# Optimization experiments

Hardware: AMD Instinct MI355X
Metric: run time of the kernel (lower is better)

Reference implementation:

```python
import jax, jax.numpy as jnp
import numpy as np

B, T, C, H = 2, 2048, 2048, 16
HD = C // H  # head dim = 128
BASE = 10000.0


def _rope_tables(seq_len, d):
    p = jnp.arange(d // 2, dtype=jnp.float32)
    # faithful to source: exponent uses 2**p (power of two), not 2*p
    theta = jnp.power(BASE, -(2.0 ** p) / d)            # [d/2]
    pos = jnp.arange(1, seq_len + 1, dtype=jnp.float32)[:, None]  # 1-indexed positions
    c = pos * theta                                      # [T, d/2]
    ang = jnp.concatenate([c, c], axis=-1)               # [T, d]
    return jnp.cos(ang), jnp.sin(ang)


def _rope(x):
    # x: [B, H, T, d]
    d = x.shape[-1]
    cos, sin = _rope_tables(x.shape[-2], d)
    half = d // 2
    x_rot = jnp.concatenate([-x[..., half:], x[..., :half]], axis=-1)
    return x * cos + x_rot * sin


def setup_inputs() -> dict:
    key = jax.random.key(0)
    k1, k2, k3 = jax.random.split(key, 3)
    x = jax.random.normal(k1, (B, T, C), dtype=jnp.float32)
    Wqkv = jax.random.normal(k2, (3 * C, C), dtype=jnp.float32) * 0.02
    bqkv = jnp.zeros((3 * C,), dtype=jnp.float32)
    Wo = jax.random.normal(k3, (C, C), dtype=jnp.float32) * 0.02
    bo = jnp.zeros((C,), dtype=jnp.float32)
    return {"x": x, "Wqkv": Wqkv, "bqkv": bqkv, "Wo": Wo, "bo": bo}


def reference(x, Wqkv, bqkv, Wo, bo):
    b, t, c = x.shape
    qkv = x @ Wqkv.T + bqkv                      # [B, T, 3C]
    q, k, v = jnp.split(qkv, 3, axis=-1)
    # [B, T, C] -> [B, H, T, HD]
    def to_heads(z):
        return z.reshape(b, t, H, HD).transpose(0, 2, 1, 3)
    q, k, v = to_heads(q), to_heads(k), to_heads(v)
    q = _rope(q)
    k = _rope(k)
    scale = 1.0 / jnp.sqrt(jnp.float32(HD))
    att = jnp.einsum('bhqd,bhkd->bhqk', q, k) * scale   # [B, H, T, T]
    causal = jnp.tril(jnp.ones((t, t), dtype=bool))
    att = jnp.where(causal, att, -jnp.inf)
    att = jax.nn.softmax(att, axis=-1)
    y = jnp.einsum('bhqk,bhkd->bhqd', att, v)           # [B, H, T, HD]
    y = y.transpose(0, 2, 1, 3).reshape(b, t, c)
    y = y @ Wo.T + bo
    return y
```

## Files before the change

### kernel.cpp

```cpp
#include <hip/hip_runtime.h>
#include <hip/hip_bf16.h>


typedef __attribute__((ext_vector_type(8))) short short8;
typedef __attribute__((ext_vector_type(4))) float f32x4;

#define B_  2
#define T_  2048
#define C_  2048
#define H_  16
#define HD_ 128

__device__ __forceinline__ float bf2f(unsigned short u) {
  union { unsigned int i; float f; } v; v.i = ((unsigned int)u) << 16; return v.f;
}
__device__ __forceinline__ unsigned short f2bf(float f) {
  union { float f; unsigned int i; } v; v.f = f;
  unsigned int x = v.i;
  return (unsigned short)((x + 0x7fffu + ((x >> 16) & 1u)) >> 16);
}
__device__ __forceinline__ float fexp2(float x) {
#if __has_builtin(__builtin_amdgcn_exp2f)
  return __builtin_amdgcn_exp2f(x);
#else
  return exp2f(x);
#endif
}

__device__ __forceinline__ void gll16(const unsigned short* g, unsigned short* lds_base) {
  __builtin_amdgcn_global_load_lds(
      (const __attribute__((address_space(1))) void*)g,
      (__attribute__((address_space(3))) void*)lds_base, 16, 0, 0);
}

__global__ void cvt_k(const float* __restrict__ src, unsigned short* __restrict__ dst, int n4)
{
  int i = blockIdx.x * blockDim.x + threadIdx.x;
  if (i < n4) {
    float4 v = ((const float4*)src)[i];
    ushort4 h;
    h.x = f2bf(v.x); h.y = f2bf(v.y); h.z = f2bf(v.z); h.w = f2bf(v.w);
    ((ushort4*)dst)[i] = h;
  }
}

template<int MODE>
__global__ __launch_bounds__(256, 2)
void gemm_bt(const unsigned short* __restrict__ A,
             const unsigned short* __restrict__ Bw,
             const float* __restrict__ bias,
             float* __restrict__ Cout,
             unsigned short* __restrict__ Qb,
             unsigned short* __restrict__ Kb,
             unsigned short* __restrict__ Vb,
             int N, int K)
{
  __shared__ unsigned short Al[128 * 64];
  __shared__ unsigned short Bl[128 * 64];
  const int tid  = threadIdx.x;
  const int wave = tid >> 6, lane = tid & 63;
  const int quad = lane >> 4, l15 = lane & 15;
  const int wm = wave >> 1, wn = wave & 1;
  const int n0 = blockIdx.x * 128, m0 = blockIdx.y * 128;

  f32x4 acc[4][4];
#pragma unroll
  for (int i = 0; i < 4; i++)
#pragma unroll
    for (int j = 0; j < 4; j++) acc[i][j] = (f32x4){0.f, 0.f, 0.f, 0.f};

  for (int k0 = 0; k0 < K; k0 += 64) {
    __syncthreads();
    const unsigned short* Ag = A + (size_t)m0 * K + k0;
    const unsigned short* Bg = Bw + (size_t)n0 * K + k0;
#pragma unroll
    for (int i = 0; i < 4; i++) {
      int cc = i * 256 + wave * 64 + lane;
      int r = cc >> 3;
      int c8 = (cc & 7) ^ (r & 7);
      gll16(Ag + (size_t)r * K + c8 * 8, &Al[(i * 4 + wave) * 512]);
      gll16(Bg + (size_t)r * K + c8 * 8, &Bl[(i * 4 + wave) * 512]);
    }
    __syncthreads();
#pragma unroll
    for (int kc = 0; kc < 2; kc++) {
      const int csw = (((kc * 4 + quad) ^ (l15 & 7)) * 8);
      short8 af[4], bfr[4];
#pragma unroll
      for (int mi = 0; mi < 4; mi++)
        af[mi] = *(const short8*)&Al[(wm * 64 + mi * 16 + l15) * 64 + csw];
#pragma unroll
      for (int ni = 0; ni < 4; ni++)
        bfr[ni] = *(const short8*)&Bl[(wn * 64 + ni * 16 + l15) * 64 + csw];
#pragma unroll
      for (int mi = 0; mi < 4; mi++)
#pragma unroll
        for (int ni = 0; ni < 4; ni++)
          acc[mi][ni] = __builtin_amdgcn_mfma_f32_16x16x32_bf16(af[mi], bfr[ni], acc[mi][ni], 0, 0, 0);
    }
  }

  if constexpr (MODE == 0) {
#pragma unroll
    for (int mi = 0; mi < 4; mi++)
#pragma unroll
      for (int ni = 0; ni < 4; ni++) {
        int col = n0 + wn * 64 + ni * 16 + l15;
        float bv = bias[col];
#pragma unroll
        for (int r = 0; r < 4; r++) {
          int row = m0 + wm * 64 + mi * 16 + quad * 4 + r;
          Cout[(size_t)row * N + col] = acc[mi][ni][r] + bv;
        }
      }
  } else {
    int which = n0 >> 11;
    int h = (n0 >> 7) & 15;
    unsigned short* P = (which == 0) ? Qb : (which == 1) ? Kb : Vb;
#pragma unroll
    for (int mi = 0; mi < 4; mi++)
#pragma unroll
      for (int ni = 0; ni < 4; ni++) {
        int d = wn * 64 + ni * 16 + l15;
        float bv = bias[n0 + d];
#pragma unroll
        for (int r = 0; r < 4; r++) {
          int m = m0 + wm * 64 + mi * 16 + quad * 4 + r;
          int b = m >> 11, t = m & (T_ - 1);
          size_t addr = (which == 2)
              ? ((size_t)((b * H_ + h) * HD_ + d)) * T_ + t
              : ((size_t)((b * H_ + h) * T_ + t)) * HD_ + d;
          P[addr] = f2bf(acc[mi][ni][r] + bv);
        }
      }
  }
}

__global__ void rope_k(unsigned short* __restrict__ Q, unsigned short* __restrict__ K)
{
  const int tid = threadIdx.x;
  const int w = tid >> 6, l = tid & 63;
  const int r = blockIdx.x * 4 + w;
  const int t = r & (T_ - 1);
  const float pos = (float)(t + 1);
  const float theta = expf(-exp2f((float)l) * 0.07195578415606394f);
  const float ang = pos * theta;
  const float c = cosf(ang), s = sinf(ang);
  const float QS = 0.08838834764831845f * 1.4426950408889634f;
  const size_t base = (size_t)r * HD_;

  float q0 = bf2f(Q[base + l]), q1 = bf2f(Q[base + l + 64]);
  Q[base + l]      = f2bf((q0 * c - q1 * s) * QS);
  Q[base + l + 64] = f2bf((q1 * c + q0 * s) * QS);
  float k0 = bf2f(K[base + l]), k1 = bf2f(K[base + l + 64]);
  K[base + l]      = f2bf(k0 * c - k1 * s);
  K[base + l + 64] = f2bf(k1 * c + k0 * s);
}

__global__ __launch_bounds__(256, 2)
void attn_k(const unsigned short* __restrict__ Q,
            const unsigned short* __restrict__ K,
            const unsigned short* __restrict__ Vt_g,
            unsigned short* __restrict__ AO)
{
  __shared__ unsigned short Kl[64 * 128];
  __shared__ unsigned short Vl[128 * 64];
  __shared__ unsigned short Pl[4 * 16 * 72];

  const int tid  = threadIdx.x;
  const int wave = tid >> 6, lane = tid & 63;
  const int quad = lane >> 4, l15 = lane & 15;
  const int blk = blockIdx.x;
  const int bh = (blk & 7) + 8 * ((blk >> 3) & 3);
  const int qp = (blk >> 5) & 15;
  const unsigned short* Qh = Q    + (size_t)bh * T_ * HD_;
  const unsigned short* Kh = K    + (size_t)bh * T_ * HD_;
  const unsigned short* Vh = Vt_g + (size_t)bh * T_ * HD_;
  const int b = bh >> 4, h = bh & 15;

#pragma unroll
  for (int tile = 0; tile < 2; tile++) {
    const int q0 = (tile == 0 ? qp : 31 - qp) * 64;
    const int wq = q0 + wave * 16;
    short8 qf[4];
#pragma unroll
    for (int kc = 0; kc < 4; kc++)
      qf[kc] = *(const short8*)&Qh[(size_t)(wq + l15) * HD_ + kc * 32 + quad * 8];

    f32x4 oacc[8];
#pragma unroll
    for (int n = 0; n < 8; n++) oacc[n] = (f32x4){0.f, 0.f, 0.f, 0.f};
    float mst[4], lst[4];
#pragma unroll
    for (int r = 0; r < 4; r++) { mst[r] = -1e30f; lst[r] = 0.f; }

    const int niter = (q0 >> 6) + 1;
    for (int it = 0; it < niter; it++) {
      const int kt = it * 64;
      __syncthreads();
#pragma unroll
      for (int i = 0; i < 4; i++) {
        int cc = i * 256 + wave * 64 + lane;
        int kr = cc >> 4, kcs = (cc & 15) ^ (kr & 15);
        gll16(Kh + (size_t)(kt + kr) * HD_ + kcs * 8, &Kl[(i * 4 + wave) * 512]);
        int vr = cc >> 3, vcs = (cc & 7) ^ (vr & 7);
        gll16(Vh + (size_t)vr * T_ + kt + vcs * 8, &Vl[(i * 4 + wave) * 512]);
      }
      __syncthreads();

      f32x4 sa[4];
#pragma unroll
      for (int ni = 0; ni < 4; ni++) sa[ni] = (f32x4){0.f, 0.f, 0.f, 0.f};
#pragma unroll
      for (int kc = 0; kc < 4; kc++) {
        const int cswK = (((kc * 4 + quad) ^ l15) * 8);
        short8 bfr[4];
#pragma unroll
        for (int ni = 0; ni < 4; ni++)
          bfr[ni] = *(const short8*)&Kl[(ni * 16 + l15) * HD_ + cswK];
#pragma unroll
        for (int ni = 0; ni < 4; ni++)
          sa[ni] = __builtin_amdgcn_mfma_f32_16x16x32_bf16(qf[kc], bfr[ni], sa[ni], 0, 0, 0);
      }

      if (kt == q0) {
#pragma unroll
        for (int ni = 0; ni < 4; ni++) {
          int gcol = kt + ni * 16 + l15;
#pragma unroll
          for (int r = 0; r < 4; r++) {
            int grow = wq + quad * 4 + r;
            if (gcol > grow) sa[ni][r] = -1e30f;
          }
        }
      }

      float rmax[4] = {-1e30f, -1e30f, -1e30f, -1e30f};
#pragma unroll
      for (int ni = 0; ni < 4; ni++)
#pragma unroll
        for (int r = 0; r < 4; r++) rmax[r] = fmaxf(rmax[r], sa[ni][r]);
#pragma unroll
      for (int r = 0; r < 4; r++)
#pragma unroll
        for (int off = 1; off < 16; off <<= 1)
          rmax[r] = fmaxf(rmax[r], __shfl_xor(rmax[r], off));
      float alpha[4];
#pragma unroll
      for (int r = 0; r < 4; r++) {
        float mnew = fmaxf(mst[r], rmax[r]);
        alpha[r] = fexp2(fminf(mst[r] - mnew, 0.f));
        mst[r] = mnew;
      }
      float rsum[4] = {0.f, 0.f, 0.f, 0.f};
#pragma unroll
      for (int ni = 0; ni < 4; ni++)
#pragma unroll
        for (int r = 0; r < 4; r++) {
          float p = fexp2(fminf(sa[ni][r] - mst[r], 0.f));
          sa[ni][r] = p;
          rsum[r] += p;
        }
#pragma unroll
      for (int r = 0; r < 4; r++) {
#pragma unroll
        for (int off = 1; off < 16; off <<= 1)
          rsum[r] += __shfl_xor(rsum[r], off);
        lst[r] = lst[r] * alpha[r] + rsum[r];
      }
#pragma unroll
      for (int nv = 0; nv < 8; nv++)
#pragma unroll
        for (int r = 0; r < 4; r++) oacc[nv][r] *= alpha[r];
#pragma unroll
      for (int ni = 0; ni < 4; ni++)
#pragma unroll
        for (int r = 0; r < 4; r++)
          Pl[wave * 16 * 72 + (quad * 4 + r) * 72 + ni * 16 + l15] = f2bf(sa[ni][r]);
      __syncthreads();

      short8 pf[2];
#pragma unroll
      for (int kc = 0; kc < 2; kc++)
        pf[kc] = *(const short8*)&Pl[wave * 16 * 72 + l15 * 72 + kc * 32 + quad * 8];
#pragma unroll
      for (int kc = 0; kc < 2; kc++) {
        const int cswV = (((kc * 4 + quad) ^ (l15 & 7)) * 8);
#pragma unroll
        for (int nv = 0; nv < 8; nv++) {
          short8 vb = *(const short8*)&Vl[(nv * 16 + l15) * 64 + cswV];
          oacc[nv] = __builtin_amdgcn_mfma_f32_16x16x32_bf16(pf[kc], vb, oacc[nv], 0, 0, 0);
        }
      }
    }

    float linv[4];
#pragma unroll
    for (int r = 0; r < 4; r++) linv[r] = 1.0f / fmaxf(lst[r], 1e-20f);
#pragma unroll
    for (int nv = 0; nv < 8; nv++)
#pragma unroll
      for (int r = 0; r < 4; r++) {
        int t = wq + quad * 4 + r;
        int d = nv * 16 + l15;
        AO[((size_t)(b * T_ + t)) * C_ + h * HD_ + d] = f2bf(oacc[nv][r] * linv[r]);
      }
  }
}

template<int A32, int B32, int MODE>
__global__ __launch_bounds__(256, 2)
void gemm_nt(const void* __restrict__ Ap, const void* __restrict__ Bp,
             const float* __restrict__ bias,
             float* __restrict__ Cout,
             unsigned short* __restrict__ Qb,
             unsigned short* __restrict__ Kb,
             unsigned short* __restrict__ Vb,
             int N, int K)
{
  __shared__ unsigned short Al[128 * 72];
  __shared__ unsigned short Bl[128 * 72];
  const int tid  = threadIdx.x;
  const int wave = tid >> 6, lane = tid & 63;
  const int quad = lane >> 4, l15 = lane & 15;
  const int wm = wave >> 1, wn = wave & 1;
  const int n0 = blockIdx.x * 128, m0 = blockIdx.y * 128;

  f32x4 acc[4][4];
#pragma unroll
  for (int i = 0; i < 4; i++)
#pragma unroll
    for (int j = 0; j < 4; j++) acc[i][j] = (f32x4){0.f, 0.f, 0.f, 0.f};

  for (int k0 = 0; k0 < K; k0 += 64) {
    __syncthreads();
    if constexpr (A32) {
      const float* A = (const float*)Ap;
#pragma unroll
      for (int i = 0; i < 8; i++) {
        int cid = tid + i * 256;
        int r = cid >> 4, c = cid & 15;
        float4 v = *(const float4*)&A[(size_t)(m0 + r) * K + k0 + c * 4];
        ushort4 hh;
        hh.x = f2bf(v.x); hh.y = f2bf(v.y); hh.z = f2bf(v.z); hh.w = f2bf(v.w);
        *(ushort4*)&Al[r * 72 + c * 4] = hh;
      }
    } else {
      const unsigned short* A = (const unsigned short*)Ap;
#pragma unroll
      for (int i = 0; i < 4; i++) {
        int cid = tid + i * 256;
        int r = cid >> 3, c = cid & 7;
        *(float4*)&Al[r * 72 + c * 8] =
            *(const float4*)&A[(size_t)(m0 + r) * K + k0 + c * 8];
      }
    }
    if constexpr (B32) {
      const float* Bm = (const float*)Bp;
#pragma unroll
      for (int i = 0; i < 8; i++) {
        int cid = tid + i * 256;
        int r = cid >> 4, c = cid & 15;
        float4 v = *(const float4*)&Bm[(size_t)(n0 + r) * K + k0 + c * 4];
        ushort4 hh;
        hh.x = f2bf(v.x); hh.y = f2bf(v.y); hh.z = f2bf(v.z); hh.w = f2bf(v.w);
        *(ushort4*)&Bl[r * 72 + c * 4] = hh;
      }
    } else {
      const unsigned short* Bm = (const unsigned short*)Bp;
#pragma unroll
      for (int i = 0; i < 4; i++) {
        int cid = tid + i * 256;
        int r = cid >> 3, c = cid & 7;
        *(float4*)&Bl[r * 72 + c * 8] =
            *(const float4*)&Bm[(size_t)(n0 + r) * K + k0 + c * 8];
      }
    }
    __syncthreads();
#pragma unroll
    for (int kc = 0; kc < 2; kc++) {
      short8 af[4], bfr[4];
#pragma unroll
      for (int mi = 0; mi < 4; mi++)
        af[mi] = *(const short8*)&Al[(wm * 64 + mi * 16 + l15) * 72 + kc * 32 + quad * 8];
#pragma unroll
      for (int ni = 0; ni < 4; ni++)
        bfr[ni] = *(const short8*)&Bl[(wn * 64 + ni * 16 + l15) * 72 + kc * 32 + quad * 8];
#pragma unroll
      for (int mi = 0; mi < 4; mi++)
#pragma unroll
        for (int ni = 0; ni < 4; ni++)
          acc[mi][ni] = __builtin_amdgcn_mfma_f32_16x16x32_bf16(af[mi], bfr[ni], acc[mi][ni], 0, 0, 0);
    }
  }

  if constexpr (MODE == 0) {
#pragma unroll
    for (int mi = 0; mi < 4; mi++)
#pragma unroll
      for (int ni = 0; ni < 4; ni++) {
        int col = n0 + wn * 64 + ni * 16 + l15;
        float bv = bias[col];
#pragma unroll
        for (int r = 0; r < 4; r++) {
          int row = m0 + wm * 64 + mi * 16 + quad * 4 + r;
          Cout[(size_t)row * N + col] = acc[mi][ni][r] + bv;
        }
      }
  } else {
    int which = n0 >> 11;
    int h = (n0 >> 7) & 15;
    unsigned short* P = (which == 0) ? Qb : (which == 1) ? Kb : Vb;
#pragma unroll
    for (int mi = 0; mi < 4; mi++)
#pragma unroll
      for (int ni = 0; ni < 4; ni++) {
        int d = wn * 64 + ni * 16 + l15;
        float bv = bias[n0 + d];
#pragma unroll
        for (int r = 0; r < 4; r++) {
          int m = m0 + wm * 64 + mi * 16 + quad * 4 + r;
          int b = m >> 11, t = m & (T_ - 1);
          size_t addr = (which == 2)
              ? ((size_t)((b * H_ + h) * HD_ + d)) * T_ + t
              : ((size_t)((b * H_ + h) * T_ + t)) * HD_ + d;
          P[addr] = f2bf(acc[mi][ni][r] + bv);
        }
      }
  }
}

extern "C" void kernel_launch(void* const* d_in, const int* in_sizes, int n_in,
                              void* d_out, int out_size, void* d_ws, size_t ws_size,
                              hipStream_t stream)
{
  const float* x    = (const float*)d_in[0];
  const float* Wqkv = (const float*)d_in[1];
  const float* bqkv = (const float*)d_in[2];
  const float* Wo   = (const float*)d_in[3];
  const float* bo   = (const float*)d_in[4];
  float* out = (float*)d_out;

  const size_t SZ   = (size_t)B_ * H_ * T_ * HD_;
  const size_t NX   = SZ;
  const size_t NWQ  = (size_t)3 * C_ * C_;
  const size_t NWO  = (size_t)C_ * C_;
  unsigned short* ws = (unsigned short*)d_ws;

  dim3 blk(256, 1, 1);
  const size_t need = (NX + NWQ + 3 * SZ) * sizeof(unsigned short);

  if (ws_size >= need) {
    unsigned short* xb    = ws;
    unsigned short* Wqkvb = xb + NX;
    unsigned short* Qb    = Wqkvb + NWQ;
    unsigned short* Kb    = Qb + SZ;
    unsigned short* Vb    = Kb + SZ;
    unsigned short* AO    = xb;
    unsigned short* Wob   = Wqkvb;

    cvt_k<<<dim3((unsigned)(NX / 1024)), blk, 0, stream>>>(x, xb, (int)(NX / 4));
    cvt_k<<<dim3((unsigned)(NWQ / 1024)), blk, 0, stream>>>(Wqkv, Wqkvb, (int)(NWQ / 4));
    gemm_bt<1><<<dim3(48, 32, 1), blk, 0, stream>>>(
        xb, Wqkvb, bqkv, nullptr, Qb, Kb, Vb, 6144, 2048);
    cvt_k<<<dim3((unsigned)(NWO / 1024)), blk, 0, stream>>>(Wo, Wob, (int)(NWO / 4));
    rope_k<<<dim3((B_ * H_ * T_) / 4, 1, 1), blk, 0, stream>>>(Qb, Kb);
    attn_k<<<dim3(512, 1, 1), blk, 0, stream>>>(Qb, Kb, Vb, AO);
    gemm_bt<0><<<dim3(16, 32, 1), blk, 0, stream>>>(
        AO, Wob, bo, out, nullptr, nullptr, nullptr, 2048, 2048);
  } else {
    unsigned short* Qb = ws;
    unsigned short* Kb = Qb + SZ;
    unsigned short* Vb = Kb + SZ;
    unsigned short* AO = Vb + SZ;
    gemm_nt<1, 1, 1><<<dim3(48, 32, 1), blk, 0, stream>>>(
        (const void*)x, (const void*)Wqkv, bqkv, nullptr, Qb, Kb, Vb, 6144, 2048);
    rope_k<<<dim3((B_ * H_ * T_) / 4, 1, 1), blk, 0, stream>>>(Qb, Kb);
    attn_k<<<dim3(512, 1, 1), blk, 0, stream>>>(Qb, Kb, Vb, AO);
    gemm_nt<0, 1, 0><<<dim3(16, 32, 1), blk, 0, stream>>>(
        (const void*)AO, (const void*)Wo, bo, out, nullptr, nullptr, nullptr, 2048, 2048);
  }
}
```

Before: 384.2 us.

## Rewrite projection GEMMs with 512-thread double-buffered async LDS pipeline and grid swizzle

Replaces the 256-thread 128x128 GEMM with a 512-thread 128x256 tile kernel that double-buffers LDS in 32-wide k halves. The next tile is prefetched via global_load_lds while MFMAs run, with manual vmcnt waits, s_setprio and raw s_barrier. A block-id swizzle groups tiles so neighbouring blocks share operand panels in L2. The aim is to hide global-load latency and cut the synchronisation stalls of the old load-sync-compute loop, in exchange for hand-managed waitcnt ordering that can break silently.

```diff
diff --git a/kernel.cpp b/kernel.cpp
--- a/kernel.cpp
+++ b/kernel.cpp
@@ -10,6 +10,15 @@
 #define C_  2048
 #define H_  16
 #define HD_ 128
+
+#define BARRIER() asm volatile("s_barrier" ::: "memory")
+#define LGKM0()   asm volatile("s_waitcnt lgkmcnt(0)" ::: "memory")
+
+template<int N> __device__ __forceinline__ void vmwait() {
+  if constexpr (N == 6)      asm volatile("s_waitcnt vmcnt(6)" ::: "memory");
+  else if constexpr (N == 3) asm volatile("s_waitcnt vmcnt(3)" ::: "memory");
+  else if constexpr (N == 0) asm volatile("s_waitcnt vmcnt(0)" ::: "memory");
+}
 
 __device__ __forceinline__ float bf2f(unsigned short u) {
   union { unsigned int i; float f; } v; v.i = ((unsigned int)u) << 16; return v.f;
@@ -44,9 +53,71 @@
   }
 }
 
+template<int CB, bool S1, bool S2, int V1, int V2>
+__device__ __forceinline__ void ktile(
+    int t,
+    const unsigned short* __restrict__ Ag,
+    const unsigned short* __restrict__ Bg, int K,
+    unsigned short (&LA)[2][2][128][32],
+    unsigned short (&LB)[2][2][256][32],
+    f32x4 (&acc)[4][4],
+    int wave, int wm, int wn, int l15, int csw8, int sra, int sc)
+{
+  short8 af[4], bf[4];
+  const int ca = sc ^ ((sra >> 1) & 3);
+
+#pragma unroll
+  for (int m = 0; m < 4; ++m)
+    af[m] = *(const short8*)&LA[CB][0][wm * 64 + m * 16 + l15][csw8];
+#pragma unroll
+  for (int n = 0; n < 4; ++n)
+    bf[n] = *(const short8*)&LB[CB][0][wn * 64 + n * 16 + l15][csw8];
+  if constexpr (S1) {
+    const int kb = (t + 1) * 64 + 32;
+    gll16(Ag + (size_t)sra * K + kb + ca * 8,         &LA[CB ^ 1][1][wave * 16][0]);
+    gll16(Bg + (size_t)sra * K + kb + ca * 8,         &LB[CB ^ 1][1][wave * 16][0]);
+    gll16(Bg + (size_t)(128 + sra) * K + kb + ca * 8, &LB[CB ^ 1][1][128 + wave * 16][0]);
+  }
+  BARRIER();
+  LGKM0();
+  __builtin_amdgcn_s_setprio(1);
+#pragma unroll
+  for (int m = 0; m < 4; ++m)
+#pragma unroll
+    for (int n = 0; n < 4; ++n)
+      acc[m][n] = __builtin_amdgcn_mfma_f32_16x16x32_bf16(af[m], bf[n], acc[m][n], 0, 0, 0);
+  __builtin_amdgcn_s_setprio(0);
+  vmwait<V1>();
+  BARRIER();
+
+#pragma unroll
+  for (int m = 0; m < 4; ++m)
+    af[m] = *(const short8*)&LA[CB][1][wm * 64 + m * 16 + l15][csw8];
+#pragma unroll
+  for (int n = 0; n < 4; ++n)
+    bf[n] = *(const short8*)&LB[CB][1][wn * 64 + n * 16 + l15][csw8];
+  if constexpr (S2) {
+    const int kb = (t + 2) * 64;
+    gll16(Ag + (size_t)sra * K + kb + ca * 8,         &LA[CB][0][wave * 16][0]);
+    gll16(Bg + (size_t)sra * K + kb + ca * 8,         &LB[CB][0][wave * 16][0]);
+    gll16(Bg + (size_t)(128 + sra) * K + kb + ca * 8, &LB[CB][0][128 + wave * 16][0]);
+  }
+  BARRIER();
+  LGKM0();
+  __builtin_amdgcn_s_setprio(1);
+#pragma unroll
+  for (int m = 0; m < 4; ++m)
+#pragma unroll
+    for (int n = 0; n < 4; ++n)
+      acc[m][n] = __builtin_amdgcn_mfma_f32_16x16x32_bf16(af[m], bf[n], acc[m][n], 0, 0, 0);
+  __builtin_amdgcn_s_setprio(0);
+  vmwait<V2>();
+  BARRIER();
+}
+
 template<int MODE>
-__global__ __launch_bounds__(256, 2)
-void gemm_bt(const unsigned short* __restrict__ A,
+__global__ __launch_bounds__(512, 2)
+void gemm128(const unsigned short* __restrict__ A,
              const unsigned short* __restrict__ Bw,
              const float* __restrict__ bias,
              float* __restrict__ Cout,
@@ -55,13 +126,25 @@
              unsigned short* __restrict__ Vb,
              int N, int K)
 {
-  __shared__ unsigned short Al[128 * 64];
-  __shared__ unsigned short Bl[128 * 64];
+  __shared__ unsigned short LA[2][2][128][32];
+  __shared__ unsigned short LB[2][2][256][32];
+
   const int tid  = threadIdx.x;
   const int wave = tid >> 6, lane = tid & 63;
   const int quad = lane >> 4, l15 = lane & 15;
-  const int wm = wave >> 1, wn = wave & 1;
-  const int n0 = blockIdx.x * 128, m0 = blockIdx.y * 128;
+  const int wm = wave >> 2, wn = wave & 3;
+  const int csw8 = (quad ^ ((l15 >> 1) & 3)) * 8;
+  const int sra = tid >> 2, sc = tid & 3;
+
+  const int ntx = N >> 8;
+  const int q8  = gridDim.x >> 3;
+  const int id  = blockIdx.x;
+  const int sw  = (id & 7) * q8 + (id >> 3);
+  const int n0  = (sw % ntx) * 256;
+  const int m0  = (sw / ntx) * 128;
+
+  const unsigned short* Ag = A  + (size_t)m0 * K;
+  const unsigned short* Bg = Bw + (size_t)n0 * K;
 
   f32x4 acc[4][4];
 #pragma unroll
@@ -69,60 +152,53 @@
 #pragma unroll
     for (int j = 0; j < 4; j++) acc[i][j] = (f32x4){0.f, 0.f, 0.f, 0.f};
 
-  for (int k0 = 0; k0 < K; k0 += 64) {
-    __syncthreads();
-    const unsigned short* Ag = A + (size_t)m0 * K + k0;
-    const unsigned short* Bg = Bw + (size_t)n0 * K + k0;
-#pragma unroll
-    for (int i = 0; i < 4; i++) {
-      int cc = i * 256 + wave * 64 + lane;
-      int r = cc >> 3;
-      int c8 = (cc & 7) ^ (r & 7);
-      gll16(Ag + (size_t)r * K + c8 * 8, &Al[(i * 4 + wave) * 512]);
-      gll16(Bg + (size_t)r * K + c8 * 8, &Bl[(i * 4 + wave) * 512]);
-    }
-    __syncthreads();
-#pragma unroll
-    for (int kc = 0; kc < 2; kc++) {
-      const int csw = (((kc * 4 + quad) ^ (l15 & 7)) * 8);
-      short8 af[4], bfr[4];
-#pragma unroll
-      for (int mi = 0; mi < 4; mi++)
-        af[mi] = *(const short8*)&Al[(wm * 64 + mi * 16 + l15) * 64 + csw];
-#pragma unroll
-      for (int ni = 0; ni < 4; ni++)
-        bfr[ni] = *(const short8*)&Bl[(wn * 64 + ni * 16 + l15) * 64 + csw];
-#pragma unroll
-      for (int mi = 0; mi < 4; mi++)
-#pragma unroll
-        for (int ni = 0; ni < 4; ni++)
-          acc[mi][ni] = __builtin_amdgcn_mfma_f32_16x16x32_bf16(af[mi], bfr[ni], acc[mi][ni], 0, 0, 0);
-    }
-  }
+  {
+    const int ca = sc ^ ((sra >> 1) & 3);
+    gll16(Ag + (size_t)sra * K + ca * 8,              &LA[0][0][wave * 16][0]);
+    gll16(Bg + (size_t)sra * K + ca * 8,              &LB[0][0][wave * 16][0]);
+    gll16(Bg + (size_t)(128 + sra) * K + ca * 8,      &LB[0][0][128 + wave * 16][0]);
+    gll16(Ag + (size_t)sra * K + 32 + ca * 8,         &LA[0][1][wave * 16][0]);
+    gll16(Bg + (size_t)sra * K + 32 + ca * 8,         &LB[0][1][wave * 16][0]);
+    gll16(Bg + (size_t)(128 + sra) * K + 32 + ca * 8, &LB[0][1][128 + wave * 16][0]);
+    gll16(Ag + (size_t)sra * K + 64 + ca * 8,         &LA[1][0][wave * 16][0]);
+    gll16(Bg + (size_t)sra * K + 64 + ca * 8,         &LB[1][0][wave * 16][0]);
+    gll16(Bg + (size_t)(128 + sra) * K + 64 + ca * 8, &LB[1][0][128 + wave * 16][0]);
+    asm volatile("s_waitcnt vmcnt(6)" ::: "memory");
+    BARRIER();
+  }
+
+  const int NT = K >> 6;
+#pragma unroll 1
+  for (int t = 0; t + 2 < NT; t += 2) {
+    ktile<0, true, true, 6, 6>(t,     Ag, Bg, K, LA, LB, acc, wave, wm, wn, l15, csw8, sra, sc);
+    ktile<1, true, true, 6, 6>(t + 1, Ag, Bg, K, LA, LB, acc, wave, wm, wn, l15, csw8, sra, sc);
+  }
+  ktile<0, true,  false, 6,  3>(NT - 2, Ag, Bg, K, LA, LB, acc, wave, wm, wn, l15, csw8, sra, sc);
+  ktile<1, false, false, 0, -1>(NT - 1, Ag, Bg, K, LA, LB, acc, wave, wm, wn, l15, csw8, sra, sc);
 
   if constexpr (MODE == 0) {
 #pragma unroll
     for (int mi = 0; mi < 4; mi++)
 #pragma unroll
-      for (int ni = 0; ni < 4; ni++) {
-        int col = n0 + wn * 64 + ni * 16 + l15;
+      for (int n = 0; n < 4; n++) {
+        int col = n0 + wn * 64 + n * 16 + l15;
         float bv = bias[col];
 #pragma unroll
         for (int r = 0; r < 4; r++) {
           int row = m0 + wm * 64 + mi * 16 + quad * 4 + r;
-          Cout[(size_t)row * N + col] = acc[mi][ni][r] + bv;
+          Cout[(size_t)row * N + col] = acc[mi][n][r] + bv;
         }
       }
   } else {
-    int which = n0 >> 11;
-    int h = (n0 >> 7) & 15;
+    const int which = n0 >> 11;
     unsigned short* P = (which == 0) ? Qb : (which == 1) ? Kb : Vb;
 #pragma unroll
     for (int mi = 0; mi < 4; mi++)
 #pragma unroll
-      for (int ni = 0; ni < 4; ni++) {
-        int d = wn * 64 + ni * 16 + l15;
-        float bv = bias[n0 + d];
+      for (int n = 0; n < 4; n++) {
+        int col = n0 + wn * 64 + n * 16 + l15;
+        float bv = bias[col];
+        int h = (col >> 7) & 15, d = col & 127;
 #pragma unroll
         for (int r = 0; r < 4; r++) {
           int m = m0 + wm * 64 + mi * 16 + quad * 4 + r;
@@ -130,7 +206,7 @@
           size_t addr = (which == 2)
               ? ((size_t)((b * H_ + h) * HD_ + d)) * T_ + t
               : ((size_t)((b * H_ + h) * T_ + t)) * HD_ + d;
-          P[addr] = f2bf(acc[mi][ni][r] + bv);
+          P[addr] = f2bf(acc[mi][n][r] + bv);
         }
       }
   }
@@ -448,6 +524,7 @@
   unsigned short* ws = (unsigned short*)d_ws;
 
   dim3 blk(256, 1, 1);
+  dim3 blk512(512, 1, 1);
   const size_t need = (NX + NWQ + 3 * SZ) * sizeof(unsigned short);
 
   if (ws_size >= need) {
@@ -461,12 +538,12 @@
 
     cvt_k<<<dim3((unsigned)(NX / 1024)), blk, 0, stream>>>(x, xb, (int)(NX / 4));
     cvt_k<<<dim3((unsigned)(NWQ / 1024)), blk, 0, stream>>>(Wqkv, Wqkvb, (int)(NWQ / 4));
-    gemm_bt<1><<<dim3(48, 32, 1), blk, 0, stream>>>(
+    gemm128<1><<<dim3(768, 1, 1), blk512, 0, stream>>>(
         xb, Wqkvb, bqkv, nullptr, Qb, Kb, Vb, 6144, 2048);
     cvt_k<<<dim3((unsigned)(NWO / 1024)), blk, 0, stream>>>(Wo, Wob, (int)(NWO / 4));
     rope_k<<<dim3((B_ * H_ * T_) / 4, 1, 1), blk, 0, stream>>>(Qb, Kb);
     attn_k<<<dim3(512, 1, 1), blk, 0, stream>>>(Qb, Kb, Vb, AO);
-    gemm_bt<0><<<dim3(16, 32, 1), blk, 0, stream>>>(
+    gemm128<0><<<dim3(256, 1, 1), blk512, 0, stream>>>(
         AO, Wob, bo, out, nullptr, nullptr, nullptr, 2048, 2048);
   } else {
     unsigned short* Qb = ws;
```

Result: slower. 435.6 us (+13.4%).

## Double-buffer K/V tiles in LDS and skip rescale when row max is unchanged

Applied to the files above, without the earlier changes.

The attention kernel now keeps two LDS buffers for K and V and prefetches the next tile with async global-to-LDS loads while computing on the current one. It synchronises with raw s_barrier and vmcnt waits instead of __syncthreads. The per-wave P staging barrier becomes an lgkmcnt wait, since each wave only reads its own P rows. The online-softmax rescale of the output accumulators is skipped when no row max grew anywhere in the wave. LDS use roughly doubles, which may reduce how many blocks fit per CU, and the hand-written waitcnt counts must match the real number of outstanding loads.

```diff
diff --git a/kernel.cpp b/kernel.cpp
--- a/kernel.cpp
+++ b/kernel.cpp
@@ -10,6 +10,14 @@
 #define C_  2048
 #define H_  16
 #define HD_ 128
+
+#define BARRIER() asm volatile("s_barrier" ::: "memory")
+#define LGKM0()   asm volatile("s_waitcnt lgkmcnt(0)" ::: "memory")
+
+template<int N> __device__ __forceinline__ void vmwait() {
+  if constexpr (N == 8)      asm volatile("s_waitcnt vmcnt(8)" ::: "memory");
+  else if constexpr (N == 0) asm volatile("s_waitcnt vmcnt(0)" ::: "memory");
+}
 
 __device__ __forceinline__ float bf2f(unsigned short u) {
   union { unsigned int i; float f; } v; v.i = ((unsigned int)u) << 16; return v.f;
@@ -163,8 +171,8 @@
             const unsigned short* __restrict__ Vt_g,
             unsigned short* __restrict__ AO)
 {
-  __shared__ unsigned short Kl[64 * 128];
-  __shared__ unsigned short Vl[128 * 64];
+  __shared__ unsigned short Kl[2][64 * 128];
+  __shared__ unsigned short Vl[2][128 * 64];
   __shared__ unsigned short Pl[4 * 16 * 72];
 
   const int tid  = threadIdx.x;
@@ -195,19 +203,37 @@
     for (int r = 0; r < 4; r++) { mst[r] = -1e30f; lst[r] = 0.f; }
 
     const int niter = (q0 >> 6) + 1;
+
+    BARRIER();
+#pragma unroll
+    for (int i = 0; i < 4; i++) {
+      int cc = i * 256 + wave * 64 + lane;
+      int kr = cc >> 4, kcs = (cc & 15) ^ (kr & 15);
+      gll16(Kh + (size_t)kr * HD_ + kcs * 8, &Kl[0][(i * 4 + wave) * 512]);
+      int vr = cc >> 3, vcs = (cc & 7) ^ (vr & 7);
+      gll16(Vh + (size_t)vr * T_ + vcs * 8, &Vl[0][(i * 4 + wave) * 512]);
+    }
+
     for (int it = 0; it < niter; it++) {
+      const int buf = it & 1;
+      BARRIER();
+      if (it + 1 < niter) {
+        const int kt1 = (it + 1) * 64;
+#pragma unroll
+        for (int i = 0; i < 4; i++) {
+          int cc = i * 256 + wave * 64 + lane;
+          int kr = cc >> 4, kcs = (cc & 15) ^ (kr & 15);
+          gll16(Kh + (size_t)(kt1 + kr) * HD_ + kcs * 8, &Kl[buf ^ 1][(i * 4 + wave) * 512]);
+          int vr = cc >> 3, vcs = (cc & 7) ^ (vr & 7);
+          gll16(Vh + (size_t)vr * T_ + kt1 + vcs * 8, &Vl[buf ^ 1][(i * 4 + wave) * 512]);
+        }
+        vmwait<8>();
+      } else {
+        vmwait<0>();
+      }
+      BARRIER();
+
       const int kt = it * 64;
-      __syncthreads();
-#pragma unroll
-      for (int i = 0; i < 4; i++) {
-        int cc = i * 256 + wave * 64 + lane;
-        int kr = cc >> 4, kcs = (cc & 15) ^ (kr & 15);
-        gll16(Kh + (size_t)(kt + kr) * HD_ + kcs * 8, &Kl[(i * 4 + wave) * 512]);
-        int vr = cc >> 3, vcs = (cc & 7) ^ (vr & 7);
-        gll16(Vh + (size_t)vr * T_ + kt + vcs * 8, &Vl[(i * 4 + wave) * 512]);
-      }
-      __syncthreads();
-
       f32x4 sa[4];
 #pragma unroll
       for (int ni = 0; ni < 4; ni++) sa[ni] = (f32x4){0.f, 0.f, 0.f, 0.f};
@@ -217,7 +243,7 @@
         short8 bfr[4];
 #pragma unroll
         for (int ni = 0; ni < 4; ni++)
-          bfr[ni] = *(const short8*)&Kl[(ni * 16 + l15) * HD_ + cswK];
+          bfr[ni] = *(const short8*)&Kl[buf][(ni * 16 + l15) * HD_ + cswK];
 #pragma unroll
         for (int ni = 0; ni < 4; ni++)
           sa[ni] = __builtin_amdgcn_mfma_f32_16x16x32_bf16(qf[kc], bfr[ni], sa[ni], 0, 0, 0);
@@ -245,19 +271,28 @@
 #pragma unroll
         for (int off = 1; off < 16; off <<= 1)
           rmax[r] = fmaxf(rmax[r], __shfl_xor(rmax[r], off));
-      float alpha[4];
-#pragma unroll
-      for (int r = 0; r < 4; r++) {
-        float mnew = fmaxf(mst[r], rmax[r]);
-        alpha[r] = fexp2(fminf(mst[r] - mnew, 0.f));
-        mst[r] = mnew;
+      int grew = (rmax[0] > mst[0]) | (rmax[1] > mst[1]) |
+                 (rmax[2] > mst[2]) | (rmax[3] > mst[3]);
+      if (__any(grew)) {
+        float alpha[4];
+#pragma unroll
+        for (int r = 0; r < 4; r++) {
+          float mnew = fmaxf(mst[r], rmax[r]);
+          alpha[r] = fexp2(mst[r] - mnew);
+          mst[r] = mnew;
+          lst[r] *= alpha[r];
+        }
+#pragma unroll
+        for (int nv = 0; nv < 8; nv++)
+#pragma unroll
+          for (int r = 0; r < 4; r++) oacc[nv][r] *= alpha[r];
       }
       float rsum[4] = {0.f, 0.f, 0.f, 0.f};
 #pragma unroll
       for (int ni = 0; ni < 4; ni++)
 #pragma unroll
         for (int r = 0; r < 4; r++) {
-          float p = fexp2(fminf(sa[ni][r] - mst[r], 0.f));
+          float p = fexp2(sa[ni][r] - mst[r]);
           sa[ni][r] = p;
           rsum[r] += p;
         }
@@ -266,18 +301,14 @@
 #pragma unroll
         for (int off = 1; off < 16; off <<= 1)
           rsum[r] += __shfl_xor(rsum[r], off);
-        lst[r] = lst[r] * alpha[r] + rsum[r];
-      }
-#pragma unroll
-      for (int nv = 0; nv < 8; nv++)
-#pragma unroll
-        for (int r = 0; r < 4; r++) oacc[nv][r] *= alpha[r];
+        lst[r] += rsum[r];
+      }
 #pragma unroll
       for (int ni = 0; ni < 4; ni++)
 #pragma unroll
         for (int r = 0; r < 4; r++)
           Pl[wave * 16 * 72 + (quad * 4 + r) * 72 + ni * 16 + l15] = f2bf(sa[ni][r]);
-      __syncthreads();
+      LGKM0();
 
       short8 pf[2];
 #pragma unroll
@@ -288,7 +319,7 @@
         const int cswV = (((kc * 4 + quad) ^ (l15 & 7)) * 8);
 #pragma unroll
         for (int nv = 0; nv < 8; nv++) {
-          short8 vb = *(const short8*)&Vl[(nv * 16 + l15) * 64 + cswV];
+          short8 vb = *(const short8*)&Vl[buf][(nv * 16 + l15) * 64 + cswV];
           oacc[nv] = __builtin_amdgcn_mfma_f32_16x16x32_bf16(pf[kc], vb, oacc[nv], 0, 0, 0);
         }
       }
```

Result: slower. 397.8 us (+3.5%).
